# Kernel optimization log

Hardware: AMD Instinct MI355X
Metric: run time of the kernel (lower is better)

Reference implementation:

```python
import jax, jax.numpy as jnp
import numpy as np
import math


def setup_inputs() -> dict:
    key = jax.random.key(0)
    k0, k1, k2, k3, k4 = jax.random.split(key, 5)
    in_f, out_f, nb = 512, 512, 8
    B, S = 4, 2048
    x = jax.random.normal(k0, (B, S, in_f), dtype=jnp.float32)
    # RBF params (frozen in original: basis_trainable=False)
    fan_in = in_f  # fan_in of rbf.weight.T which is (num_basis, in_features)
    bound = 1.0 / math.sqrt(fan_in)
    rbf_weight = jax.random.uniform(k1, (in_f, nb), dtype=jnp.float32,
                                    minval=-math.sqrt(3.0) * 0.33 / math.sqrt(fan_in),
                                    maxval=math.sqrt(3.0) * 0.33 / math.sqrt(fan_in))
    rbf_centers = jnp.tile(jnp.linspace(-bound, bound, nb, dtype=jnp.float32)[None, :], (in_f, 1))
    # KAN spline weight (in, nb, out); fan_in for init is in_f*nb
    fan2 = in_f * nb
    wb = math.sqrt(3.0) * 0.33 / math.sqrt(fan2)
    weight = jax.random.uniform(k2, (in_f, nb, out_f), dtype=jnp.float32, minval=-wb, maxval=wb)
    bias = jax.random.uniform(k3, (out_f,), dtype=jnp.float32,
                              minval=-1.0 / math.sqrt(fan2), maxval=1.0 / math.sqrt(fan2))
    scale_base = jax.random.uniform(k4, (in_f, out_f), dtype=jnp.float32, minval=-0.1, maxval=0.1)
    return {"x": x, "rbf_weight": rbf_weight, "rbf_centers": rbf_centers,
            "weight": weight, "bias": bias, "scale_base": scale_base}


def reference(x, rbf_weight, rbf_centers, weight, bias, scale_base):
    in_f = x.shape[-1]
    nb = rbf_weight.shape[1]
    beta = (nb / math.log2(nb)) ** 2  # get_rbf_width(2/nb, log2(nb))
    batch_shape = x.shape[:-1]
    xf = x.reshape(-1, in_f)  # (N, in)
    # RBF basis expansion: (N, in, nb)
    z = xf[:, :, None] * rbf_weight[None, :, :] - rbf_centers[None, :, :]
    phi = jnp.exp(-beta * (z * z))
    # spline contraction + base path, expressed as efficient contractions
    y = jnp.einsum('nib,ibo->no', phi, weight)
    y = y + bias + jnp.cos(xf) @ scale_base
    return y.reshape(*batch_shape, weight.shape[-1])
```

## Files before the change

### kernel.cpp

```cpp
#include <hip/hip_runtime.h>
#include <hip/hip_bf16.h>

typedef __attribute__((ext_vector_type(8))) short short8;
typedef __attribute__((ext_vector_type(4))) float f32x4;

#define IN_F 512
#define OUT_F 512
#define BM 128
#define BN 512
#define BK 64
#define THREADS 512
#define PHI_STEPS 64
#define NSTEPS 72
#define IMG_CHUNKS 4096
#define A_SH (BM * BK)
#define B_SH (BN * BK)
#define PART_ELEMS (8192 * OUT_F)

__device__ __forceinline__ short f2bf(float f) {
  __hip_bfloat16 h = __float2bfloat16(f);
  return __builtin_bit_cast(short, h);
}

__device__ __forceinline__ void glds16(const void* g, void* l) {
  __builtin_amdgcn_global_load_lds(
      (const __attribute__((address_space(1))) unsigned int*)g,
      (__attribute__((address_space(3))) unsigned int*)l, 16, 0, 0);
}

__device__ __forceinline__ float bsrc(const float* __restrict__ w,
                                      const float* __restrict__ sb,
                                      int k, int col) {
  return (k < IN_F * 8) ? w[(size_t)k * OUT_F + col]
                        : sb[(size_t)(k - IN_F * 8) * OUT_F + col];
}

__global__ void __launch_bounds__(256) prep_b(const float* __restrict__ w,
                                              const float* __restrict__ sb,
                                              short* __restrict__ img) {
  const int D = blockIdx.x * 256 + threadIdx.x;
  const int ci = D & (IMG_CHUNKS - 1);
  const int s = D >> 12;
  const int n = ci >> 3, slot = ci & 7;
  const int oct = slot ^ (n & 7);
  short8 v;
#pragma unroll
  for (int j = 0; j < 8; ++j) v[j] = f2bf(bsrc(w, sb, s * 64 + oct * 8 + j, n));
  *(short8*)&img[(size_t)D * 8] = v;
}

template <int NPLANES>
__global__ void __launch_bounds__(256) reduce_add(const float* __restrict__ part,
                                                  float* __restrict__ out) {
  const int n4 = PART_ELEMS / 4;
  const float4* p0 = (const float4*)part;
  const float4* p1 = (const float4*)(part + PART_ELEMS);
  const float4* p2 = (const float4*)(part + 2 * (size_t)PART_ELEMS);
  float4* o4 = (float4*)out;
  for (int i = blockIdx.x * 256 + threadIdx.x; i < n4; i += gridDim.x * 256) {
    float4 a = o4[i];
    const float4 b = p0[i];
    a.x += b.x; a.y += b.y; a.z += b.z; a.w += b.w;
    if (NPLANES >= 2) {
      const float4 c = p1[i];
      a.x += c.x; a.y += c.y; a.z += c.z; a.w += c.w;
    }
    if (NPLANES >= 3) {
      const float4 d = p2[i];
      a.x += d.x; a.y += d.y; a.z += d.z; a.w += d.w;
    }
    o4[i] = a;
  }
}

template <int KS, bool PREB>
__global__ void __launch_bounds__(THREADS, 2) kan_main(
    const float* __restrict__ x, const float* __restrict__ rw,
    const float* __restrict__ rc, const float* __restrict__ w,
    const float* __restrict__ bias, const float* __restrict__ sb,
    const short* __restrict__ bimg, float* __restrict__ out,
    float* __restrict__ part) {
  constexpr int SPLC = NSTEPS / KS;
  __shared__ __align__(16) short A_lds[2][A_SH];
  __shared__ __align__(16) short B_lds[2][B_SH];

  const int t = threadIdx.x, lane = t & 63, wid = t >> 6;
  const int wm = wid >> 2;
  const int wn = wid & 3;
  const int l15 = lane & 15, kb = lane >> 4;
  const int m0 = blockIdx.x * BM;
  const int ks = (KS > 1) ? blockIdx.y : 0;
  const int s0 = ks * SPLC;

  const int a_il = t & 7;
  const int a_m = t >> 3;
  const float c2 = -10.2591705f;

  f32x4 acc[4][8];
#pragma unroll
  for (int i = 0; i < 4; ++i)
#pragma unroll
    for (int j = 0; j < 8; ++j) acc[i][j] = (f32x4){0.f, 0.f, 0.f, 0.f};

  float xrA, xrB;
  float4 pr0, pr1, pc0, pc1;
  float4 cA0, cA1, cB0, cB1;

  auto loadNext = [&](int s1) {
    if (s1 < PHI_STEPS) {
      const int feat = s1 * 8 + a_il;
      xrA = x[(size_t)(m0 + a_m) * IN_F + feat];
      xrB = x[(size_t)(m0 + a_m + 64) * IN_F + feat];
      pr0 = *(const float4*)(rw + feat * 8);
      pr1 = *(const float4*)(rw + feat * 8 + 4);
      pc0 = *(const float4*)(rc + feat * 8);
      pc1 = *(const float4*)(rc + feat * 8 + 4);
    } else {
      const float* xpA = x + (size_t)(m0 + a_m) * IN_F + (s1 - PHI_STEPS) * 64 + a_il * 8;
      const float* xpB = xpA + (size_t)64 * IN_F;
      cA0 = *(const float4*)xpA; cA1 = *(const float4*)(xpA + 4);
      cB0 = *(const float4*)xpB; cB1 = *(const float4*)(xpB + 4);
    }
  };

  auto writeA = [&](int s1, short* __restrict__ Ad) {
    short8 avA, avB;
    if (s1 < PHI_STEPS) {
      const float rwv[8] = {pr0.x, pr0.y, pr0.z, pr0.w, pr1.x, pr1.y, pr1.z, pr1.w};
      const float rcv[8] = {pc0.x, pc0.y, pc0.z, pc0.w, pc1.x, pc1.y, pc1.z, pc1.w};
#pragma unroll
      for (int b = 0; b < 8; ++b) {
        const float zA = fmaf(xrA, rwv[b], -rcv[b]);
        const float zB = fmaf(xrB, rwv[b], -rcv[b]);
        avA[b] = f2bf(exp2f(c2 * zA * zA));
        avB[b] = f2bf(exp2f(c2 * zB * zB));
      }
    } else {
      avA[0] = f2bf(__cosf(cA0.x)); avA[1] = f2bf(__cosf(cA0.y));
      avA[2] = f2bf(__cosf(cA0.z)); avA[3] = f2bf(__cosf(cA0.w));
      avA[4] = f2bf(__cosf(cA1.x)); avA[5] = f2bf(__cosf(cA1.y));
      avA[6] = f2bf(__cosf(cA1.z)); avA[7] = f2bf(__cosf(cA1.w));
      avB[0] = f2bf(__cosf(cB0.x)); avB[1] = f2bf(__cosf(cB0.y));
      avB[2] = f2bf(__cosf(cB0.z)); avB[3] = f2bf(__cosf(cB0.w));
      avB[4] = f2bf(__cosf(cB1.x)); avB[5] = f2bf(__cosf(cB1.y));
      avB[6] = f2bf(__cosf(cB1.z)); avB[7] = f2bf(__cosf(cB1.w));
    }
    const int mA = a_m, mB = a_m + 64;
    *(short8*)&Ad[mA * BK + (a_il ^ (mA & 7)) * 8] = avA;
    *(short8*)&Ad[mB * BK + (a_il ^ (mB & 7)) * 8] = avB;
  };

  auto stageB = [&](int s, short* __restrict__ Bd) {
    if (PREB) {
      const short* src = bimg + ((size_t)s * IMG_CHUNKS + t) * 8;
#pragma unroll
      for (int c = 0; c < 8; ++c)
        glds16(src + (size_t)c * 512 * 8, Bd + c * 4096 + wid * 512);
    } else {
#pragma unroll
      for (int c = 0; c < 8; ++c) {
        const int ci = c * 512 + t;
        const int n = ci >> 3, slot = ci & 7, oct = slot ^ (n & 7);
        short8 v;
#pragma unroll
        for (int j = 0; j < 8; ++j) v[j] = f2bf(bsrc(w, sb, s * 64 + oct * 8 + j, n));
        *(short8*)&Bd[ci * 8] = v;
      }
    }
  };

  auto mfma_half = [&](const short* __restrict__ Ab, const short* __restrict__ Bb,
                       int kk) {
    const int sk = kk * 4 + kb;
    short8 af[4], bf[8];
#pragma unroll
    for (int mi = 0; mi < 4; ++mi) {
      const int r = wm * 64 + mi * 16 + l15;
      af[mi] = *(const short8*)&Ab[r * BK + (sk ^ (r & 7)) * 8];
    }
#pragma unroll
    for (int ni = 0; ni < 8; ++ni) {
      const int n = wn * 128 + ni * 16 + l15;
      bf[ni] = *(const short8*)&Bb[n * BK + (sk ^ (n & 7)) * 8];
    }
#pragma unroll
    for (int mi = 0; mi < 4; ++mi)
#pragma unroll
      for (int ni = 0; ni < 8; ++ni)
        acc[mi][ni] = __builtin_amdgcn_mfma_f32_16x16x32_bf16(
            af[mi], bf[ni], acc[mi][ni], 0, 0, 0);
  };

  stageB(s0, B_lds[0]);
  loadNext(s0);
  writeA(s0, A_lds[0]);
  __syncthreads();

  for (int si = 0; si < SPLC; ++si) {
    const int c = si & 1;
    const int s = s0 + si;
    if (si + 1 < SPLC) { stageB(s + 1, B_lds[c ^ 1]); loadNext(s + 1); }
    mfma_half(A_lds[c], B_lds[c], 0);
    if (si + 1 < SPLC) writeA(s + 1, A_lds[c ^ 1]);
    mfma_half(A_lds[c], B_lds[c], 1);
    __syncthreads();
  }

#pragma unroll
  for (int ni = 0; ni < 8; ++ni) {
    const int col = wn * 128 + ni * 16 + l15;
    const float bb = (KS == 1 || ks == 0) ? bias[col] : 0.f;
#pragma unroll
    for (int mi = 0; mi < 4; ++mi) {
      const int rb = m0 + wm * 64 + mi * 16 + kb * 4;
#pragma unroll
      for (int r4 = 0; r4 < 4; ++r4) {
        const size_t idx = (size_t)(rb + r4) * OUT_F + col;
        if (KS == 1 || ks == 0) out[idx] = acc[mi][ni][r4] + bb;
        else                    part[(size_t)(ks - 1) * PART_ELEMS + idx] = acc[mi][ni][r4];
      }
    }
  }
}

extern "C" void kernel_launch(void* const* d_in, const int* in_sizes, int n_in,
                              void* d_out, int out_size, void* d_ws, size_t ws_size,
                              hipStream_t stream) {
  const float* x    = (const float*)d_in[0];
  const float* rw   = (const float*)d_in[1];
  const float* rc   = (const float*)d_in[2];
  const float* w    = (const float*)d_in[3];
  const float* bias = (const float*)d_in[4];
  const float* sb   = (const float*)d_in[5];
  float* out = (float*)d_out;

  const int nrows = in_sizes[0] / IN_F;
  const int mb = nrows / BM;

  const size_t img_bytes  = (size_t)NSTEPS * IMG_CHUNKS * 16;
  const size_t part_bytes = (size_t)PART_ELEMS * sizeof(float);
  const int img_chunks_total = NSTEPS * IMG_CHUNKS;

  if (ws_size >= img_bytes + 3 * part_bytes) {
    short* img = (short*)d_ws;
    float* part = (float*)((char*)d_ws + img_bytes);
    prep_b<<<img_chunks_total / 256, 256, 0, stream>>>(w, sb, img);
    kan_main<4, true><<<dim3(mb, 4), THREADS, 0, stream>>>(x, rw, rc, w, bias, sb,
                                                           img, out, part);
    reduce_add<3><<<2048, 256, 0, stream>>>(part, out);
  } else if (ws_size >= img_bytes + part_bytes) {
    short* img = (short*)d_ws;
    float* part = (float*)((char*)d_ws + img_bytes);
    prep_b<<<img_chunks_total / 256, 256, 0, stream>>>(w, sb, img);
    kan_main<2, true><<<dim3(mb, 2), THREADS, 0, stream>>>(x, rw, rc, w, bias, sb,
                                                           img, out, part);
    reduce_add<1><<<2048, 256, 0, stream>>>(part, out);
  } else if (ws_size >= part_bytes) {
    float* part = (float*)d_ws;
    kan_main<2, false><<<dim3(mb, 2), THREADS, 0, stream>>>(x, rw, rc, w, bias, sb,
                                                            nullptr, out, part);
    reduce_add<1><<<2048, 256, 0, stream>>>(part, out);
  } else {
    kan_main<1, false><<<dim3(mb, 1), THREADS, 0, stream>>>(x, rw, rc, w, bias, sb,
                                                            nullptr, out, nullptr);
  }
}
```

Baseline: 83.79 us.

## Shrink block tile to 64x256, add N-tiling, reduce K-split to two

Changes the GEMM block tile from 128x512 with 512 threads to 64x256 with 256 threads. It adds an N-tile grid dimension and cuts the K-split from four to two, so the reduction pass reads one partial plane instead of three. It also replaces the bf16 conversion intrinsic with a manual round-to-nearest-even bit trick. The grid gets more, smaller blocks with less partial-sum traffic, but each block has lower MFMA reuse and recomputes the phi/cos A-tile once per N-tile, doubling the exp work.

Result: slower. 99.16 us (+18.3%).

```diff
diff --git a/kernel.cpp b/kernel.cpp
--- a/kernel.cpp
+++ b/kernel.cpp
@@ -6,20 +6,23 @@
 
 #define IN_F 512
 #define OUT_F 512
-#define BM 128
-#define BN 512
+#define BM 64
+#define BN 256
 #define BK 64
-#define THREADS 512
+#define THREADS 256
 #define PHI_STEPS 64
 #define NSTEPS 72
-#define IMG_CHUNKS 4096
+#define NT 2
+#define KSPLIT 2
+#define IMG_CHUNKS 2048
 #define A_SH (BM * BK)
 #define B_SH (BN * BK)
 #define PART_ELEMS (8192 * OUT_F)
 
 __device__ __forceinline__ short f2bf(float f) {
-  __hip_bfloat16 h = __float2bfloat16(f);
-  return __builtin_bit_cast(short, h);
+  unsigned u = __builtin_bit_cast(unsigned, f);
+  u += 0x7fffu + ((u >> 16) & 1u);
+  return (short)(u >> 16);
 }
 
 __device__ __forceinline__ void glds16(const void* g, void* l) {
@@ -40,35 +43,27 @@
                                               short* __restrict__ img) {
   const int D = blockIdx.x * 256 + threadIdx.x;
   const int ci = D & (IMG_CHUNKS - 1);
-  const int s = D >> 12;
+  const int im = D >> 11;
+  const int s = im % NSTEPS;
+  const int nt = im / NSTEPS;
   const int n = ci >> 3, slot = ci & 7;
   const int oct = slot ^ (n & 7);
+  const int col = nt * BN + n;
   short8 v;
 #pragma unroll
-  for (int j = 0; j < 8; ++j) v[j] = f2bf(bsrc(w, sb, s * 64 + oct * 8 + j, n));
+  for (int j = 0; j < 8; ++j) v[j] = f2bf(bsrc(w, sb, s * 64 + oct * 8 + j, col));
   *(short8*)&img[(size_t)D * 8] = v;
 }
 
-template <int NPLANES>
 __global__ void __launch_bounds__(256) reduce_add(const float* __restrict__ part,
                                                   float* __restrict__ out) {
   const int n4 = PART_ELEMS / 4;
-  const float4* p0 = (const float4*)part;
-  const float4* p1 = (const float4*)(part + PART_ELEMS);
-  const float4* p2 = (const float4*)(part + 2 * (size_t)PART_ELEMS);
+  const float4* p4 = (const float4*)part;
   float4* o4 = (float4*)out;
   for (int i = blockIdx.x * 256 + threadIdx.x; i < n4; i += gridDim.x * 256) {
     float4 a = o4[i];
-    const float4 b = p0[i];
+    const float4 b = p4[i];
     a.x += b.x; a.y += b.y; a.z += b.z; a.w += b.w;
-    if (NPLANES >= 2) {
-      const float4 c = p1[i];
-      a.x += c.x; a.y += c.y; a.z += c.z; a.w += c.w;
-    }
-    if (NPLANES >= 3) {
-      const float4 d = p2[i];
-      a.x += d.x; a.y += d.y; a.z += d.z; a.w += d.w;
-    }
     o4[i] = a;
   }
 }
@@ -85,22 +80,21 @@
   __shared__ __align__(16) short B_lds[2][B_SH];
 
   const int t = threadIdx.x, lane = t & 63, wid = t >> 6;
-  const int wm = wid >> 2;
-  const int wn = wid & 3;
   const int l15 = lane & 15, kb = lane >> 4;
   const int m0 = blockIdx.x * BM;
-  const int ks = (KS > 1) ? blockIdx.y : 0;
+  const int nt = blockIdx.y, n0 = nt * BN;
+  const int ks = (KS > 1) ? blockIdx.z : 0;
   const int s0 = ks * SPLC;
 
   const int a_il = t & 7;
   const int a_m = t >> 3;
   const float c2 = -10.2591705f;
 
-  f32x4 acc[4][8];
+  f32x4 acc[4][4];
 #pragma unroll
   for (int i = 0; i < 4; ++i)
 #pragma unroll
-    for (int j = 0; j < 8; ++j) acc[i][j] = (f32x4){0.f, 0.f, 0.f, 0.f};
+    for (int j = 0; j < 4; ++j) acc[i][j] = (f32x4){0.f, 0.f, 0.f, 0.f};
 
   float xrA, xrB;
   float4 pr0, pr1, pc0, pc1;
@@ -110,14 +104,14 @@
     if (s1 < PHI_STEPS) {
       const int feat = s1 * 8 + a_il;
       xrA = x[(size_t)(m0 + a_m) * IN_F + feat];
-      xrB = x[(size_t)(m0 + a_m + 64) * IN_F + feat];
+      xrB = x[(size_t)(m0 + a_m + 32) * IN_F + feat];
       pr0 = *(const float4*)(rw + feat * 8);
       pr1 = *(const float4*)(rw + feat * 8 + 4);
       pc0 = *(const float4*)(rc + feat * 8);
       pc1 = *(const float4*)(rc + feat * 8 + 4);
     } else {
       const float* xpA = x + (size_t)(m0 + a_m) * IN_F + (s1 - PHI_STEPS) * 64 + a_il * 8;
-      const float* xpB = xpA + (size_t)64 * IN_F;
+      const float* xpB = xpA + (size_t)32 * IN_F;
       cA0 = *(const float4*)xpA; cA1 = *(const float4*)(xpA + 4);
       cB0 = *(const float4*)xpB; cB1 = *(const float4*)(xpB + 4);
     }
@@ -145,25 +139,26 @@
       avB[4] = f2bf(__cosf(cB1.x)); avB[5] = f2bf(__cosf(cB1.y));
       avB[6] = f2bf(__cosf(cB1.z)); avB[7] = f2bf(__cosf(cB1.w));
     }
-    const int mA = a_m, mB = a_m + 64;
+    const int mA = a_m, mB = a_m + 32;
     *(short8*)&Ad[mA * BK + (a_il ^ (mA & 7)) * 8] = avA;
     *(short8*)&Ad[mB * BK + (a_il ^ (mB & 7)) * 8] = avB;
   };
 
   auto stageB = [&](int s, short* __restrict__ Bd) {
     if (PREB) {
-      const short* src = bimg + ((size_t)s * IMG_CHUNKS + t) * 8;
+      const short* src = bimg + ((size_t)(nt * NSTEPS + s) * IMG_CHUNKS + t) * 8;
 #pragma unroll
       for (int c = 0; c < 8; ++c)
-        glds16(src + (size_t)c * 512 * 8, Bd + c * 4096 + wid * 512);
+        glds16(src + (size_t)c * 256 * 8, Bd + c * 2048 + wid * 512);
     } else {
 #pragma unroll
       for (int c = 0; c < 8; ++c) {
-        const int ci = c * 512 + t;
+        const int ci = c * 256 + t;
         const int n = ci >> 3, slot = ci & 7, oct = slot ^ (n & 7);
         short8 v;
 #pragma unroll
-        for (int j = 0; j < 8; ++j) v[j] = f2bf(bsrc(w, sb, s * 64 + oct * 8 + j, n));
+        for (int j = 0; j < 8; ++j)
+          v[j] = f2bf(bsrc(w, sb, s * 64 + oct * 8 + j, n0 + n));
         *(short8*)&Bd[ci * 8] = v;
       }
     }
@@ -172,21 +167,21 @@
   auto mfma_half = [&](const short* __restrict__ Ab, const short* __restrict__ Bb,
                        int kk) {
     const int sk = kk * 4 + kb;
-    short8 af[4], bf[8];
+    short8 af[4], bf[4];
 #pragma unroll
     for (int mi = 0; mi < 4; ++mi) {
-      const int r = wm * 64 + mi * 16 + l15;
+      const int r = mi * 16 + l15;
       af[mi] = *(const short8*)&Ab[r * BK + (sk ^ (r & 7)) * 8];
     }
 #pragma unroll
-    for (int ni = 0; ni < 8; ++ni) {
-      const int n = wn * 128 + ni * 16 + l15;
+    for (int ni = 0; ni < 4; ++ni) {
+      const int n = wid * 64 + ni * 16 + l15;
       bf[ni] = *(const short8*)&Bb[n * BK + (sk ^ (n & 7)) * 8];
     }
 #pragma unroll
     for (int mi = 0; mi < 4; ++mi)
 #pragma unroll
-      for (int ni = 0; ni < 8; ++ni)
+      for (int ni = 0; ni < 4; ++ni)
         acc[mi][ni] = __builtin_amdgcn_mfma_f32_16x16x32_bf16(
             af[mi], bf[ni], acc[mi][ni], 0, 0, 0);
   };
@@ -207,17 +202,17 @@
   }
 
 #pragma unroll
-  for (int ni = 0; ni < 8; ++ni) {
-    const int col = wn * 128 + ni * 16 + l15;
+  for (int ni = 0; ni < 4; ++ni) {
+    const int col = n0 + wid * 64 + ni * 16 + l15;
     const float bb = (KS == 1 || ks == 0) ? bias[col] : 0.f;
 #pragma unroll
     for (int mi = 0; mi < 4; ++mi) {
-      const int rb = m0 + wm * 64 + mi * 16 + kb * 4;
+      const int rb = m0 + mi * 16 + kb * 4;
 #pragma unroll
       for (int r4 = 0; r4 < 4; ++r4) {
         const size_t idx = (size_t)(rb + r4) * OUT_F + col;
         if (KS == 1 || ks == 0) out[idx] = acc[mi][ni][r4] + bb;
-        else                    part[(size_t)(ks - 1) * PART_ELEMS + idx] = acc[mi][ni][r4];
+        else                    part[idx] = acc[mi][ni][r4];
       }
     }
   }
@@ -237,31 +232,27 @@
   const int nrows = in_sizes[0] / IN_F;
   const int mb = nrows / BM;
 
-  const size_t img_bytes  = (size_t)NSTEPS * IMG_CHUNKS * 16;
+  const size_t img_bytes  = (size_t)NT * NSTEPS * IMG_CHUNKS * 16;
   const size_t part_bytes = (size_t)PART_ELEMS * sizeof(float);
-  const int img_chunks_total = NSTEPS * IMG_CHUNKS;
-
-  if (ws_size >= img_bytes + 3 * part_bytes) {
+  const int img_chunks_total = NT * NSTEPS * IMG_CHUNKS;
+
+  if (ws_size >= img_bytes + part_bytes) {
     short* img = (short*)d_ws;
     float* part = (float*)((char*)d_ws + img_bytes);
     prep_b<<<img_chunks_total / 256, 256, 0, stream>>>(w, sb, img);
-    kan_main<4, true><<<dim3(mb, 4), THREADS, 0, stream>>>(x, rw, rc, w, bias, sb,
-                                                           img, out, part);
-    reduce_add<3><<<2048, 256, 0, stream>>>(part, out);
-  } else if (ws_size >= img_bytes + part_bytes) {
-    short* img = (short*)d_ws;
-    float* part = (float*)((char*)d_ws + img_bytes);
-    prep_b<<<img_chunks_total / 256, 256, 0, stream>>>(w, sb, img);
-    kan_main<2, true><<<dim3(mb, 2), THREADS, 0, stream>>>(x, rw, rc, w, bias, sb,
-                                                           img, out, part);
-    reduce_add<1><<<2048, 256, 0, stream>>>(part, out);
+    dim3 grid(mb, NT, KSPLIT);
+    kan_main<KSPLIT, true><<<grid, THREADS, 0, stream>>>(x, rw, rc, w, bias, sb,
+                                                         img, out, part);
+    reduce_add<<<2048, 256, 0, stream>>>(part, out);
   } else if (ws_size >= part_bytes) {
     float* part = (float*)d_ws;
-    kan_main<2, false><<<dim3(mb, 2), THREADS, 0, stream>>>(x, rw, rc, w, bias, sb,
-                                                            nullptr, out, part);
-    reduce_add<1><<<2048, 256, 0, stream>>>(part, out);
+    dim3 grid(mb, NT, KSPLIT);
+    kan_main<KSPLIT, false><<<grid, THREADS, 0, stream>>>(x, rw, rc, w, bias, sb,
+                                                          nullptr, out, part);
+    reduce_add<<<2048, 256, 0, stream>>>(part, out);
   } else {
-    kan_main<1, false><<<dim3(mb, 1), THREADS, 0, stream>>>(x, rw, rc, w, bias, sb,
-                                                            nullptr, out, nullptr);
-  }
-}
+    dim3 grid(mb, NT, 1);
+    kan_main<1, false><<<grid, THREADS, 0, stream>>>(x, rw, rc, w, bias, sb,
+                                                     nullptr, out, nullptr);
+  }
+}
```

## Stagger phi generation and MFMA across wave pairs with deeper x prefetch

Applied to the files above, without the earlier changes.

Reorders the main loop so even waves write the next A tile before their MFMAs and odd waves write it after, with s_setprio raised around the MFMA blocks. The intent is to overlap transcendental VALU work with matrix math across waves. x values for the phi steps are now prefetched two steps ahead in double-buffered registers, and the cos-path loads move into writeA. bf16 conversion is replaced by a manual round-to-nearest-even bit trick, which drops NaN handling. This adds register pressure and makes the cos-step loads exposed rather than prefetched.

Measured after the change: 92.52 us. 10.4% more time.

```diff
diff --git a/kernel.cpp b/kernel.cpp
--- a/kernel.cpp
+++ b/kernel.cpp
@@ -18,8 +18,9 @@
 #define PART_ELEMS (8192 * OUT_F)
 
 __device__ __forceinline__ short f2bf(float f) {
-  __hip_bfloat16 h = __float2bfloat16(f);
-  return __builtin_bit_cast(short, h);
+  unsigned u = __builtin_bit_cast(unsigned, f);
+  u += 0x7fffu + ((u >> 16) & 1u);
+  return (short)(u >> 16);
 }
 
 __device__ __forceinline__ void glds16(const void* g, void* l) {
@@ -102,48 +103,50 @@
 #pragma unroll
     for (int j = 0; j < 8; ++j) acc[i][j] = (f32x4){0.f, 0.f, 0.f, 0.f};
 
-  float xrA, xrB;
+  float xA0, xB0, xA1, xB1;
   float4 pr0, pr1, pc0, pc1;
-  float4 cA0, cA1, cB0, cB1;
-
-  auto loadNext = [&](int s1) {
-    if (s1 < PHI_STEPS) {
-      const int feat = s1 * 8 + a_il;
-      xrA = x[(size_t)(m0 + a_m) * IN_F + feat];
-      xrB = x[(size_t)(m0 + a_m + 64) * IN_F + feat];
-      pr0 = *(const float4*)(rw + feat * 8);
-      pr1 = *(const float4*)(rw + feat * 8 + 4);
-      pc0 = *(const float4*)(rc + feat * 8);
-      pc1 = *(const float4*)(rc + feat * 8 + 4);
-    } else {
-      const float* xpA = x + (size_t)(m0 + a_m) * IN_F + (s1 - PHI_STEPS) * 64 + a_il * 8;
-      const float* xpB = xpA + (size_t)64 * IN_F;
-      cA0 = *(const float4*)xpA; cA1 = *(const float4*)(xpA + 4);
-      cB0 = *(const float4*)xpB; cB1 = *(const float4*)(xpB + 4);
-    }
-  };
-
-  auto writeA = [&](int s1, short* __restrict__ Ad) {
+
+  auto loadXphi = [&](int s2, int set) {
+    const int feat = s2 * 8 + a_il;
+    const float v1 = x[(size_t)(m0 + a_m) * IN_F + feat];
+    const float v2 = x[(size_t)(m0 + a_m + 64) * IN_F + feat];
+    if (set == 0) { xA0 = v1; xB0 = v2; } else { xA1 = v1; xB1 = v2; }
+  };
+  auto loadPar = [&](int s1) {
+    const int feat = s1 * 8 + a_il;
+    pr0 = *(const float4*)(rw + feat * 8);
+    pr1 = *(const float4*)(rw + feat * 8 + 4);
+    pc0 = *(const float4*)(rc + feat * 8);
+    pc1 = *(const float4*)(rc + feat * 8 + 4);
+  };
+
+  auto writeA = [&](int s1, int set, short* __restrict__ Ad) {
     short8 avA, avB;
     if (s1 < PHI_STEPS) {
+      const float xa = (set == 0) ? xA0 : xA1;
+      const float xb = (set == 0) ? xB0 : xB1;
       const float rwv[8] = {pr0.x, pr0.y, pr0.z, pr0.w, pr1.x, pr1.y, pr1.z, pr1.w};
       const float rcv[8] = {pc0.x, pc0.y, pc0.z, pc0.w, pc1.x, pc1.y, pc1.z, pc1.w};
 #pragma unroll
       for (int b = 0; b < 8; ++b) {
-        const float zA = fmaf(xrA, rwv[b], -rcv[b]);
-        const float zB = fmaf(xrB, rwv[b], -rcv[b]);
+        const float zA = fmaf(xa, rwv[b], -rcv[b]);
+        const float zB = fmaf(xb, rwv[b], -rcv[b]);
         avA[b] = f2bf(exp2f(c2 * zA * zA));
         avB[b] = f2bf(exp2f(c2 * zB * zB));
       }
     } else {
-      avA[0] = f2bf(__cosf(cA0.x)); avA[1] = f2bf(__cosf(cA0.y));
-      avA[2] = f2bf(__cosf(cA0.z)); avA[3] = f2bf(__cosf(cA0.w));
-      avA[4] = f2bf(__cosf(cA1.x)); avA[5] = f2bf(__cosf(cA1.y));
-      avA[6] = f2bf(__cosf(cA1.z)); avA[7] = f2bf(__cosf(cA1.w));
-      avB[0] = f2bf(__cosf(cB0.x)); avB[1] = f2bf(__cosf(cB0.y));
-      avB[2] = f2bf(__cosf(cB0.z)); avB[3] = f2bf(__cosf(cB0.w));
-      avB[4] = f2bf(__cosf(cB1.x)); avB[5] = f2bf(__cosf(cB1.y));
-      avB[6] = f2bf(__cosf(cB1.z)); avB[7] = f2bf(__cosf(cB1.w));
+      const float* xpA = x + (size_t)(m0 + a_m) * IN_F + (s1 - PHI_STEPS) * 64 + a_il * 8;
+      const float* xpB = xpA + (size_t)64 * IN_F;
+      const float4 u0 = *(const float4*)xpA, u1 = *(const float4*)(xpA + 4);
+      const float4 v0 = *(const float4*)xpB, v1 = *(const float4*)(xpB + 4);
+      avA[0] = f2bf(__cosf(u0.x)); avA[1] = f2bf(__cosf(u0.y));
+      avA[2] = f2bf(__cosf(u0.z)); avA[3] = f2bf(__cosf(u0.w));
+      avA[4] = f2bf(__cosf(u1.x)); avA[5] = f2bf(__cosf(u1.y));
+      avA[6] = f2bf(__cosf(u1.z)); avA[7] = f2bf(__cosf(u1.w));
+      avB[0] = f2bf(__cosf(v0.x)); avB[1] = f2bf(__cosf(v0.y));
+      avB[2] = f2bf(__cosf(v0.z)); avB[3] = f2bf(__cosf(v0.w));
+      avB[4] = f2bf(__cosf(v1.x)); avB[5] = f2bf(__cosf(v1.y));
+      avB[6] = f2bf(__cosf(v1.z)); avB[7] = f2bf(__cosf(v1.w));
     }
     const int mA = a_m, mB = a_m + 64;
     *(short8*)&Ad[mA * BK + (a_il ^ (mA & 7)) * 8] = avA;
@@ -192,17 +195,35 @@
   };
 
   stageB(s0, B_lds[0]);
-  loadNext(s0);
-  writeA(s0, A_lds[0]);
+  loadXphi(s0, 0);
+  loadPar(s0);
+  writeA(s0, 0, A_lds[0]);
+  loadXphi(s0 + 1, 1);
   __syncthreads();
 
   for (int si = 0; si < SPLC; ++si) {
     const int c = si & 1;
     const int s = s0 + si;
-    if (si + 1 < SPLC) { stageB(s + 1, B_lds[c ^ 1]); loadNext(s + 1); }
-    mfma_half(A_lds[c], B_lds[c], 0);
-    if (si + 1 < SPLC) writeA(s + 1, A_lds[c ^ 1]);
-    mfma_half(A_lds[c], B_lds[c], 1);
+    const bool more = (si + 1 < SPLC);
+    if (more) {
+      stageB(s + 1, B_lds[c ^ 1]);
+      if (si + 2 < SPLC && (s + 2) < PHI_STEPS) loadXphi(s + 2, c);
+      if ((s + 1) < PHI_STEPS) loadPar(s + 1);
+    }
+    __builtin_amdgcn_sched_barrier(0);
+    if ((wid & 1) == 0) {
+      if (more) writeA(s + 1, (si + 1) & 1, A_lds[c ^ 1]);
+      __builtin_amdgcn_s_setprio(1);
+      mfma_half(A_lds[c], B_lds[c], 0);
+      mfma_half(A_lds[c], B_lds[c], 1);
+      __builtin_amdgcn_s_setprio(0);
+    } else {
+      __builtin_amdgcn_s_setprio(1);
+      mfma_half(A_lds[c], B_lds[c], 0);
+      mfma_half(A_lds[c], B_lds[c], 1);
+      __builtin_amdgcn_s_setprio(0);
+      if (more) writeA(s + 1, (si + 1) & 1, A_lds[c ^ 1]);
+    }
     __syncthreads();
   }
 
```
